# Performance work log

Hardware: AMD Instinct MI355X
Metric: run time of the kernel (lower is better)

Reference implementation:

```python
import jax, jax.numpy as jnp
import numpy as np

ALPHA = 1.5      # entmax alpha (q parameter)
N_ITER = 50      # entmax-bisect iterations (entmax library default)
B, S, DM, H, HKV, HD = 1, 2048, 2048, 16, 4, 128
ROPE_THETA = 10000.0


def _entmax_p(x):
    """alpha-entmax along last axis via bisection on tau (matches entmax.EntmaxBisect)."""
    am1 = ALPHA - 1.0
    pw = 1.0 / am1
    X = x * am1
    d = x.shape[-1]
    max_val = jnp.max(X, axis=-1, keepdims=True)
    tau_lo = max_val - 1.0                      # _gp(1, alpha) = 1
    tau_hi = max_val - (1.0 / d) ** am1          # _gp(1/d, alpha)
    dm0 = tau_hi - tau_lo

    def body(i, carry):
        tau_lo, dm, tau_m = carry
        dm = dm * 0.5
        tau_m = tau_lo + dm
        p = jnp.maximum(X - tau_m, 0.0) ** pw
        f = jnp.sum(p, axis=-1, keepdims=True) - 1.0
        tau_lo = jnp.where(f >= 0, tau_m, tau_lo)
        return (tau_lo, dm, tau_m)

    tau_lo, dm, tau_m = jax.lax.fori_loop(0, N_ITER, body, (tau_lo, dm0, tau_lo))
    p = jnp.maximum(X - tau_m, 0.0) ** pw
    return p / jnp.sum(p, axis=-1, keepdims=True)  # ensure_sum_one


@jax.custom_vjp
def entmax_bisect(x):
    return _entmax_p(x)

def _emx_fwd(x):
    p = _entmax_p(x)
    return p, p

def _emx_bwd(p, g):
    # entmax library backward: gppr = p^(2-alpha) on support
    gppr = jnp.where(p > 0, p ** (2.0 - ALPHA), 0.0)
    dX = g * gppr
    q = jnp.sum(dX, axis=-1, keepdims=True) / jnp.sum(gppr, axis=-1, keepdims=True)
    return ((dX - q * gppr),)

entmax_bisect.defvjp(_emx_fwd, _emx_bwd)


def _rotate_half(x):
    x1, x2 = x[..., : HD // 2], x[..., HD // 2:]
    return jnp.concatenate([-x2, x1], axis=-1)


def setup_inputs() -> dict:
    key = jax.random.key(0)
    k1, k2, k3, k4, k5 = jax.random.split(key, 5)
    hidden_states = jax.random.normal(k1, (B, S, DM), dtype=jnp.float32)
    wq = jax.random.normal(k2, (H * HD, DM), dtype=jnp.float32) * 0.02
    wk = jax.random.normal(k3, (HKV * HD, DM), dtype=jnp.float32) * 0.02
    wv = jax.random.normal(k4, (HKV * HD, DM), dtype=jnp.float32) * 0.02
    wo = jax.random.normal(k5, (DM, H * HD), dtype=jnp.float32) * 0.02
    # real Llama RoPE position embeddings
    inv_freq = 1.0 / (ROPE_THETA ** (np.arange(0, HD, 2, dtype=np.float32) / HD))
    pos = np.arange(S, dtype=np.float32)
    freqs = pos[:, None] * inv_freq[None, :]          # [S, HD/2]
    emb = np.concatenate([freqs, freqs], axis=-1)     # [S, HD]
    cos = jnp.asarray(np.cos(emb))[None]              # [1, S, HD]
    sin = jnp.asarray(np.sin(emb))[None]
    return {"hidden_states": hidden_states, "cos": cos, "sin": sin,
            "wq": wq, "wk": wk, "wv": wv, "wo": wo}


def reference(hidden_states, cos, sin, wq, wk, wv, wo):
    b, s, _ = hidden_states.shape
    scaling = HD ** -0.5
    # QKV projections -> [B, H, S, HD]
    q = (hidden_states @ wq.T).reshape(b, s, H, HD).transpose(0, 2, 1, 3)
    k = (hidden_states @ wk.T).reshape(b, s, HKV, HD).transpose(0, 2, 1, 3)
    v = (hidden_states @ wv.T).reshape(b, s, HKV, HD).transpose(0, 2, 1, 3)
    # RoPE (cos/sin broadcast over head axis)
    c, sn = cos[:, None, :, :], sin[:, None, :, :]
    q = q * c + _rotate_half(q) * sn
    k = k * c + _rotate_half(k) * sn
    # GQA: repeat kv heads
    g = H // HKV
    k = jnp.repeat(k, g, axis=1)
    v = jnp.repeat(v, g, axis=1)
    scores = jnp.einsum('bhqd,bhkd->bhqk', q, k) * scaling
    causal = jnp.tril(jnp.ones((s, s), dtype=bool))
    scores = jnp.where(causal, scores, -jnp.inf)
    attn = entmax_bisect(scores)                      # [B, H, S, S]
    out = jnp.einsum('bhqk,bhkd->bhqd', attn, v)
    out = out.transpose(0, 2, 1, 3).reshape(b, s, H * HD)
    out = out @ wo.T
    return (out, attn)
```

## Files before the change

### kernel.cpp

```cpp
#include <hip/hip_runtime.h>

typedef __bf16 bf16;
typedef __bf16 bf16x4 __attribute__((ext_vector_type(4)));
typedef __bf16 bf16x8 __attribute__((ext_vector_type(8)));
typedef float f32x4 __attribute__((ext_vector_type(4)));

#define S 2048
#define DM 2048
#define HD 128
#define H 16
#define NQKV 3072
#define N_ITER_DEV 32

__device__ __forceinline__ void gl2lds16(const void* g, void* l) {
    __builtin_amdgcn_global_load_lds(
        (const __attribute__((address_space(1))) void*)g,
        (__attribute__((address_space(3))) void*)l, 16, 0, 0);
}

__global__ void cvt4_kernel(const float* __restrict__ in, bf16* __restrict__ out, int n4) {
    int i = blockIdx.x * blockDim.x + threadIdx.x;
    if (i < n4) {
        float4 f = ((const float4*)in)[i];
        bf16x4 o;
        o[0] = (bf16)f.x; o[1] = (bf16)f.y; o[2] = (bf16)f.z; o[3] = (bf16)f.w;
        ((bf16x4*)out)[i] = o;
    }
}

__global__ __launch_bounds__(256) void gemm128_bt(const bf16* __restrict__ A,
                                                  const bf16* __restrict__ B,
                                                  float* __restrict__ C, int Ndim, int K) {
    __shared__ bf16 As[128 * 32];
    __shared__ bf16 Bs[128 * 32];
    int m0 = blockIdx.x * 128, n0 = blockIdx.y * 128;
    int t = threadIdx.x;
    int l = t & 63, w = t >> 6;
    int lane16 = l & 15, quad = l >> 4;

    int c0 = (w * 2) * 64 + l;
    int c1 = c0 + 64;
    const bf16* Abase = A + (size_t)m0 * K;
    const bf16* Bbase = B + (size_t)n0 * K;

    int wm = (w & 1) * 64, wn = (w >> 1) * 64;
    f32x4 acc[4][4];
#pragma unroll
    for (int i = 0; i < 4; i++)
#pragma unroll
        for (int j = 0; j < 4; j++) acc[i][j] = (f32x4){0.f, 0.f, 0.f, 0.f};

    for (int k0 = 0; k0 < K; k0 += 32) {
        gl2lds16(Abase + (size_t)(c0 >> 2) * K + k0 + (c0 & 3) * 8, &As[(w * 2) * 512]);
        gl2lds16(Abase + (size_t)(c1 >> 2) * K + k0 + (c1 & 3) * 8, &As[(w * 2 + 1) * 512]);
        gl2lds16(Bbase + (size_t)(c0 >> 2) * K + k0 + (c0 & 3) * 8, &Bs[(w * 2) * 512]);
        gl2lds16(Bbase + (size_t)(c1 >> 2) * K + k0 + (c1 & 3) * 8, &Bs[(w * 2 + 1) * 512]);
        __syncthreads();
        bf16x8 af[4], bfr[4];
#pragma unroll
        for (int i = 0; i < 4; i++)
            af[i] = *(const bf16x8*)&As[(wm + i * 16 + lane16) * 32 + quad * 8];
#pragma unroll
        for (int j = 0; j < 4; j++)
            bfr[j] = *(const bf16x8*)&Bs[(wn + j * 16 + lane16) * 32 + quad * 8];
#pragma unroll
        for (int i = 0; i < 4; i++)
#pragma unroll
            for (int j = 0; j < 4; j++)
                acc[i][j] = __builtin_amdgcn_mfma_f32_16x16x32_bf16(af[i], bfr[j], acc[i][j], 0, 0, 0);
        __syncthreads();
    }
#pragma unroll
    for (int i = 0; i < 4; i++)
#pragma unroll
        for (int j = 0; j < 4; j++) {
            float* cp = C + (size_t)(m0 + wm + i * 16 + quad * 4) * Ndim + n0 + wn + j * 16 + lane16;
#pragma unroll
            for (int r = 0; r < 4; r++) cp[(size_t)r * Ndim] = acc[i][j][r];
        }
}

__global__ void rope_kernel(const float* __restrict__ qkv, const float* __restrict__ cosb,
                            const float* __restrict__ sinb, bf16* __restrict__ qs,
                            bf16* __restrict__ kb, bf16* __restrict__ vT) {
    int col = blockIdx.x * 256 + threadIdx.x;
    int s = blockIdx.y;
    const float* row = qkv + (size_t)s * NQKV;
    float v = row[col];
    if (col < DM) {
        int h = col >> 7, d = col & 127;
        float c = cosb[s * HD + d], sn = sinb[s * HD + d];
        float other = row[(h << 7) + ((d < 64) ? (d + 64) : (d - 64))];
        float rot = (d < 64) ? -other : other;
        float o = v * c + rot * sn;
        qs[((size_t)h * S + s) * HD + d] = (bf16)(o * 0.04419417382415922f);
    } else if (col < DM + 512) {
        int c2 = col - DM;
        int kv = c2 >> 7, d = c2 & 127;
        float c = cosb[s * HD + d], sn = sinb[s * HD + d];
        float other = row[DM + (kv << 7) + ((d < 64) ? (d + 64) : (d - 64))];
        float rot = (d < 64) ? -other : other;
        float o = v * c + rot * sn;
        kb[((size_t)kv * S + s) * HD + d] = (bf16)o;
    } else {
        int c2 = col - DM - 512;
        int kv = c2 >> 7, d = c2 & 127;
        vT[((size_t)kv * HD + d) * S + s] = (bf16)v;
    }
}

template <int SEGS>
__global__ __launch_bounds__(1024) void attn_kernel(const bf16* __restrict__ qs,
                                                    const bf16* __restrict__ kb,
                                                    float* __restrict__ attn, int bx_base) {
    constexpr int NREG = SEGS * 8;
    __shared__ float sc[16][528];
    int bx = bx_base + blockIdx.x;
    int h = blockIdx.y;
    int r0 = bx * 16;
    int jlen = r0 + 16;
    int l = threadIdx.x & 63;
    int w = threadIdx.x >> 6;
    int lane16 = l & 15, quad = l >> 4;

    const bf16* qrow = qs + ((size_t)h * S + (r0 + lane16)) * HD + quad * 8;
    bf16x8 afrag[4];
#pragma unroll
    for (int kc = 0; kc < 4; kc++) afrag[kc] = *(const bf16x8*)(qrow + kc * 32);

    const bf16* kbase = kb + (size_t)(h >> 2) * S * HD;
    float xr[NREG];
    int my_i = r0 + w;

#pragma unroll
    for (int sgi = 0; sgi < SEGS; sgi++) {
        int j0 = sgi * 512;
#pragma unroll
        for (int tt = 0; tt < 2; tt++) {
            int t = w + tt * 16;
            int jt = j0 + t * 16;
            if (jt < jlen) {
                f32x4 acc = {0.f, 0.f, 0.f, 0.f};
                const bf16* kp = kbase + (size_t)(jt + lane16) * HD + quad * 8;
#pragma unroll
                for (int kc = 0; kc < 4; kc++) {
                    bf16x8 b = *(const bf16x8*)(kp + kc * 32);
                    acc = __builtin_amdgcn_mfma_f32_16x16x32_bf16(afrag[kc], b, acc, 0, 0, 0);
                }
                int jj = jt + lane16;
#pragma unroll
                for (int r = 0; r < 4; r++) {
                    int rowi = quad * 4 + r;
                    float v = acc[r];
                    if (jj > r0 + rowi) v = -1e30f;
                    sc[rowi][t * 16 + lane16] = v;
                }
            }
        }
        __syncthreads();
#pragma unroll
        for (int c = 0; c < 8; c++) {
            int j = j0 + c * 64 + l;
            xr[sgi * 8 + c] = (j < jlen) ? sc[w][c * 64 + l] : -1e30f;
        }
        __syncthreads();
    }

    float m = -1e30f;
#pragma unroll
    for (int c = 0; c < NREG; c++) m = fmaxf(m, xr[c]);
#pragma unroll
    for (int off = 1; off < 64; off <<= 1) m = fmaxf(m, __shfl_xor(m, off));

    float tau_lo = m - 1.0f;
    float dm = 0.97790291309f;
    float tau_m = tau_lo;
    for (int it = 0; it < N_ITER_DEV; it++) {
        dm *= 0.5f;
        tau_m = tau_lo + dm;
        float f = 0.f;
#pragma unroll
        for (int c = 0; c < NREG; c++) {
            float t = fmaxf(xr[c] - tau_m, 0.f);
            f = fmaf(t, t, f);
        }
#pragma unroll
        for (int off = 1; off < 64; off <<= 1) f += __shfl_xor(f, off);
        tau_lo = (f >= 1.0f) ? tau_m : tau_lo;
    }

    float ssum = 0.f;
#pragma unroll
    for (int c = 0; c < NREG; c++) {
        float t = fmaxf(xr[c] - tau_m, 0.f);
        ssum = fmaf(t, t, ssum);
    }
#pragma unroll
    for (int off = 1; off < 64; off <<= 1) ssum += __shfl_xor(ssum, off);
    float inv = 1.0f / ssum;

    float* arow = attn + ((size_t)h * S + my_i) * S;
#pragma unroll
    for (int c = 0; c < NREG; c++) {
        float t = fmaxf(xr[c] - tau_m, 0.f);
        arow[c * 64 + l] = t * t * inv;
    }
    for (int j = SEGS * 512 + l; j < S; j += 64) arow[j] = 0.f;
}

__global__ __launch_bounds__(256) void av128(const float* __restrict__ attn,
                                             const bf16* __restrict__ vT,
                                             bf16* __restrict__ o) {
    __shared__ bf16 As[64 * 32];
    __shared__ bf16 Bs[128 * 32];
    int m0 = blockIdx.x * 64;
    int h = blockIdx.y;
    int t = threadIdx.x, l = t & 63, w = t >> 6;
    int lane16 = l & 15, quad = l >> 4;
    const float* Abase = attn + ((size_t)h * S + m0) * S;
    const bf16* Bbase = vT + (size_t)(h >> 2) * HD * S;
    int wm = (w & 1) * 32, wn = (w >> 1) * 64;
    f32x4 acc[2][4];
#pragma unroll
    for (int i = 0; i < 2; i++)
#pragma unroll
        for (int j = 0; j < 4; j++) acc[i][j] = (f32x4){0.f, 0.f, 0.f, 0.f};

    int ar = t >> 2, ac = (t & 3) * 8;
    int cB0 = (w * 2) * 64 + l, cB1 = cB0 + 64;
    int Kv = m0 + 64;

    for (int k0 = 0; k0 < Kv; k0 += 32) {
        float4 f0 = *(const float4*)(Abase + (size_t)ar * S + k0 + ac);
        float4 f1 = *(const float4*)(Abase + (size_t)ar * S + k0 + ac + 4);
        bf16x8 a8;
        a8[0] = (bf16)f0.x; a8[1] = (bf16)f0.y; a8[2] = (bf16)f0.z; a8[3] = (bf16)f0.w;
        a8[4] = (bf16)f1.x; a8[5] = (bf16)f1.y; a8[6] = (bf16)f1.z; a8[7] = (bf16)f1.w;
        *(bf16x8*)&As[ar * 32 + ac] = a8;
        gl2lds16(Bbase + (size_t)(cB0 >> 2) * S + k0 + (cB0 & 3) * 8, &Bs[(w * 2) * 512]);
        gl2lds16(Bbase + (size_t)(cB1 >> 2) * S + k0 + (cB1 & 3) * 8, &Bs[(w * 2 + 1) * 512]);
        __syncthreads();
        bf16x8 af[2], bfr[4];
#pragma unroll
        for (int i = 0; i < 2; i++)
            af[i] = *(const bf16x8*)&As[(wm + i * 16 + lane16) * 32 + quad * 8];
#pragma unroll
        for (int j = 0; j < 4; j++)
            bfr[j] = *(const bf16x8*)&Bs[(wn + j * 16 + lane16) * 32 + quad * 8];
#pragma unroll
        for (int i = 0; i < 2; i++)
#pragma unroll
            for (int j = 0; j < 4; j++)
                acc[i][j] = __builtin_amdgcn_mfma_f32_16x16x32_bf16(af[i], bfr[j], acc[i][j], 0, 0, 0);
        __syncthreads();
    }
#pragma unroll
    for (int i = 0; i < 2; i++)
#pragma unroll
        for (int j = 0; j < 4; j++) {
            bf16* op = o + (size_t)(m0 + wm + i * 16 + quad * 4) * DM + h * HD + wn + j * 16 + lane16;
#pragma unroll
            for (int r = 0; r < 4; r++) op[(size_t)r * DM] = (bf16)acc[i][j][r];
        }
}

extern "C" void kernel_launch(void* const* d_in, const int* in_sizes, int n_in,
                              void* d_out, int out_size, void* d_ws, size_t ws_size,
                              hipStream_t stream) {
    const float* hidden = (const float*)d_in[0];
    const float* cosb   = (const float*)d_in[1];
    const float* sinb   = (const float*)d_in[2];
    const float* wq     = (const float*)d_in[3];
    const float* wk     = (const float*)d_in[4];
    const float* wv     = (const float*)d_in[5];
    const float* wo     = (const float*)d_in[6];
    char* ws = (char*)d_ws;
    bf16*  bf_hidden = (bf16*)(ws);
    bf16*  bf_wqkv   = (bf16*)(ws + 8388608);
    bf16*  bf_wo     = (bf16*)(ws + 20971520);
    float* qkv_raw   = (float*)(ws + 29360128);
    bf16*  qsb       = (bf16*)(ws + 54525952);
    bf16*  kbb       = (bf16*)(ws + 62914560);
    bf16*  vTb       = (bf16*)(ws + 65011712);
    float* out  = (float*)d_out;
    float* attn = out + 4194304;

    cvt4_kernel<<<dim3(4096), 256, 0, stream>>>(hidden, bf_hidden, 1048576);
    cvt4_kernel<<<dim3(4096), 256, 0, stream>>>(wq, bf_wqkv, 1048576);
    cvt4_kernel<<<dim3(1024), 256, 0, stream>>>(wk, bf_wqkv + 2048 * 2048, 262144);
    cvt4_kernel<<<dim3(1024), 256, 0, stream>>>(wv, bf_wqkv + 2048 * 2048 + 512 * 2048, 262144);
    cvt4_kernel<<<dim3(4096), 256, 0, stream>>>(wo, bf_wo, 1048576);

    gemm128_bt<<<dim3(16, 24), 256, 0, stream>>>(bf_hidden, bf_wqkv, qkv_raw, NQKV, DM);

    rope_kernel<<<dim3(12, S), 256, 0, stream>>>(qkv_raw, cosb, sinb, qsb, kbb, vTb);

    attn_kernel<1><<<dim3(32, H), 1024, 0, stream>>>(qsb, kbb, attn, 0);
    attn_kernel<2><<<dim3(32, H), 1024, 0, stream>>>(qsb, kbb, attn, 32);
    attn_kernel<3><<<dim3(32, H), 1024, 0, stream>>>(qsb, kbb, attn, 64);
    attn_kernel<4><<<dim3(32, H), 1024, 0, stream>>>(qsb, kbb, attn, 96);

    av128<<<dim3(32, H), 256, 0, stream>>>(attn, vTb, bf_hidden);

    gemm128_bt<<<dim3(16, 16), 256, 0, stream>>>(bf_hidden, bf_wo, out, DM, DM);
}
```

Before: 693.9 us.

## Fuse attention-times-V into entmax attention kernel and merge conversion launches

```diff
diff --git a/kernel.cpp b/kernel.cpp
--- a/kernel.cpp
+++ b/kernel.cpp
@@ -18,14 +18,23 @@
         (__attribute__((address_space(3))) void*)l, 16, 0, 0);
 }
 
-__global__ void cvt4_kernel(const float* __restrict__ in, bf16* __restrict__ out, int n4) {
+__global__ void cvt_all(const float* __restrict__ hid, const float* __restrict__ wq,
+                        const float* __restrict__ wk, const float* __restrict__ wv,
+                        const float* __restrict__ wo, bf16* __restrict__ bh,
+                        bf16* __restrict__ bqkv, bf16* __restrict__ bwo) {
     int i = blockIdx.x * blockDim.x + threadIdx.x;
-    if (i < n4) {
-        float4 f = ((const float4*)in)[i];
-        bf16x4 o;
-        o[0] = (bf16)f.x; o[1] = (bf16)f.y; o[2] = (bf16)f.z; o[3] = (bf16)f.w;
-        ((bf16x4*)out)[i] = o;
-    }
+    const float* src;
+    bf16* dst;
+    int off;
+    if (i < 1048576) { src = hid; dst = bh; off = i; }
+    else if (i < 2097152) { src = wq; dst = bqkv; off = i - 1048576; }
+    else if (i < 2359296) { src = wk; dst = bqkv + 2048 * 2048; off = i - 2097152; }
+    else if (i < 2621440) { src = wv; dst = bqkv + 2048 * 2048 + 512 * 2048; off = i - 2359296; }
+    else { src = wo; dst = bwo; off = i - 2621440; }
+    float4 f = ((const float4*)src)[off];
+    bf16x4 o;
+    o[0] = (bf16)f.x; o[1] = (bf16)f.y; o[2] = (bf16)f.z; o[3] = (bf16)f.w;
+    ((bf16x4*)dst)[off] = o;
 }
 
 __global__ __launch_bounds__(256) void gemm128_bt(const bf16* __restrict__ A,
@@ -110,11 +119,14 @@
 }
 
 template <int SEGS>
-__global__ __launch_bounds__(1024) void attn_kernel(const bf16* __restrict__ qs,
-                                                    const bf16* __restrict__ kb,
-                                                    float* __restrict__ attn, int bx_base) {
+__global__ __launch_bounds__(1024) void attn_av_kernel(const bf16* __restrict__ qs,
+                                                       const bf16* __restrict__ kb,
+                                                       const bf16* __restrict__ vT,
+                                                       float* __restrict__ attn,
+                                                       bf16* __restrict__ o, int bx_base) {
     constexpr int NREG = SEGS * 8;
     __shared__ float sc[16][528];
+    __shared__ bf16 pb[16][552];
     int bx = bx_base + blockIdx.x;
     int h = blockIdx.y;
     int r0 = bx * 16;
@@ -129,6 +141,7 @@
     for (int kc = 0; kc < 4; kc++) afrag[kc] = *(const bf16x8*)(qrow + kc * 32);
 
     const bf16* kbase = kb + (size_t)(h >> 2) * S * HD;
+    const bf16* vbase = vT + (size_t)(h >> 2) * HD * S;
     float xr[NREG];
     int my_i = r0 + w;
 
@@ -173,11 +186,11 @@
     for (int off = 1; off < 64; off <<= 1) m = fmaxf(m, __shfl_xor(m, off));
 
     float tau_lo = m - 1.0f;
-    float dm = 0.97790291309f;
+    float dmh = 0.97790291309f;
     float tau_m = tau_lo;
     for (int it = 0; it < N_ITER_DEV; it++) {
-        dm *= 0.5f;
-        tau_m = tau_lo + dm;
+        dmh *= 0.5f;
+        tau_m = tau_lo + dmh;
         float f = 0.f;
 #pragma unroll
         for (int c = 0; c < NREG; c++) {
@@ -200,68 +213,46 @@
     float inv = 1.0f / ssum;
 
     float* arow = attn + ((size_t)h * S + my_i) * S;
-#pragma unroll
-    for (int c = 0; c < NREG; c++) {
-        float t = fmaxf(xr[c] - tau_m, 0.f);
-        arow[c * 64 + l] = t * t * inv;
-    }
+    int jt_o = (w & 7) * 16;
+    int kh = (w >> 3) * 256;
+    f32x4 acc_o = {0.f, 0.f, 0.f, 0.f};
+
+#pragma unroll
+    for (int sgi = 0; sgi < SEGS; sgi++) {
+        int j0 = sgi * 512;
+#pragma unroll
+        for (int c = 0; c < 8; c++) {
+            float t = fmaxf(xr[sgi * 8 + c] - tau_m, 0.f);
+            float p = t * t * inv;
+            arow[j0 + c * 64 + l] = p;
+            pb[w][c * 64 + l] = (bf16)p;
+        }
+        __syncthreads();
+#pragma unroll
+        for (int ks = 0; ks < 8; ks++) {
+            int kk = kh + ks * 32;
+            bf16x8 a = *(const bf16x8*)&pb[lane16][kk + quad * 8];
+            bf16x8 b = *(const bf16x8*)(vbase + (size_t)(jt_o + lane16) * S + j0 + kk + quad * 8);
+            acc_o = __builtin_amdgcn_mfma_f32_16x16x32_bf16(a, b, acc_o, 0, 0, 0);
+        }
+        __syncthreads();
+    }
+
     for (int j = SEGS * 512 + l; j < S; j += 64) arow[j] = 0.f;
-}
-
-__global__ __launch_bounds__(256) void av128(const float* __restrict__ attn,
-                                             const bf16* __restrict__ vT,
-                                             bf16* __restrict__ o) {
-    __shared__ bf16 As[64 * 32];
-    __shared__ bf16 Bs[128 * 32];
-    int m0 = blockIdx.x * 64;
-    int h = blockIdx.y;
-    int t = threadIdx.x, l = t & 63, w = t >> 6;
-    int lane16 = l & 15, quad = l >> 4;
-    const float* Abase = attn + ((size_t)h * S + m0) * S;
-    const bf16* Bbase = vT + (size_t)(h >> 2) * HD * S;
-    int wm = (w & 1) * 32, wn = (w >> 1) * 64;
-    f32x4 acc[2][4];
-#pragma unroll
-    for (int i = 0; i < 2; i++)
-#pragma unroll
-        for (int j = 0; j < 4; j++) acc[i][j] = (f32x4){0.f, 0.f, 0.f, 0.f};
-
-    int ar = t >> 2, ac = (t & 3) * 8;
-    int cB0 = (w * 2) * 64 + l, cB1 = cB0 + 64;
-    int Kv = m0 + 64;
-
-    for (int k0 = 0; k0 < Kv; k0 += 32) {
-        float4 f0 = *(const float4*)(Abase + (size_t)ar * S + k0 + ac);
-        float4 f1 = *(const float4*)(Abase + (size_t)ar * S + k0 + ac + 4);
-        bf16x8 a8;
-        a8[0] = (bf16)f0.x; a8[1] = (bf16)f0.y; a8[2] = (bf16)f0.z; a8[3] = (bf16)f0.w;
-        a8[4] = (bf16)f1.x; a8[5] = (bf16)f1.y; a8[6] = (bf16)f1.z; a8[7] = (bf16)f1.w;
-        *(bf16x8*)&As[ar * 32 + ac] = a8;
-        gl2lds16(Bbase + (size_t)(cB0 >> 2) * S + k0 + (cB0 & 3) * 8, &Bs[(w * 2) * 512]);
-        gl2lds16(Bbase + (size_t)(cB1 >> 2) * S + k0 + (cB1 & 3) * 8, &Bs[(w * 2 + 1) * 512]);
-        __syncthreads();
-        bf16x8 af[2], bfr[4];
-#pragma unroll
-        for (int i = 0; i < 2; i++)
-            af[i] = *(const bf16x8*)&As[(wm + i * 16 + lane16) * 32 + quad * 8];
-#pragma unroll
-        for (int j = 0; j < 4; j++)
-            bfr[j] = *(const bf16x8*)&Bs[(wn + j * 16 + lane16) * 32 + quad * 8];
-#pragma unroll
-        for (int i = 0; i < 2; i++)
-#pragma unroll
-            for (int j = 0; j < 4; j++)
-                acc[i][j] = __builtin_amdgcn_mfma_f32_16x16x32_bf16(af[i], bfr[j], acc[i][j], 0, 0, 0);
-        __syncthreads();
-    }
-#pragma unroll
-    for (int i = 0; i < 2; i++)
-#pragma unroll
-        for (int j = 0; j < 4; j++) {
-            bf16* op = o + (size_t)(m0 + wm + i * 16 + quad * 4) * DM + h * HD + wn + j * 16 + lane16;
-#pragma unroll
-            for (int r = 0; r < 4; r++) op[(size_t)r * DM] = (bf16)acc[i][j][r];
-        }
+
+    if (w >= 8) {
+#pragma unroll
+        for (int r = 0; r < 4; r++) sc[w - 8][l * 4 + r] = acc_o[r];
+    }
+    __syncthreads();
+    if (w < 8) {
+        bf16* op = o + (size_t)(r0 + quad * 4) * DM + h * HD + jt_o + lane16;
+#pragma unroll
+        for (int r = 0; r < 4; r++) {
+            float v = acc_o[r] + sc[w][l * 4 + r];
+            op[(size_t)r * DM] = (bf16)v;
+        }
+    }
 }
 
 extern "C" void kernel_launch(void* const* d_in, const int* in_sizes, int n_in,
@@ -285,22 +276,16 @@
     float* out  = (float*)d_out;
     float* attn = out + 4194304;
 
-    cvt4_kernel<<<dim3(4096), 256, 0, stream>>>(hidden, bf_hidden, 1048576);
-    cvt4_kernel<<<dim3(4096), 256, 0, stream>>>(wq, bf_wqkv, 1048576);
-    cvt4_kernel<<<dim3(1024), 256, 0, stream>>>(wk, bf_wqkv + 2048 * 2048, 262144);
-    cvt4_kernel<<<dim3(1024), 256, 0, stream>>>(wv, bf_wqkv + 2048 * 2048 + 512 * 2048, 262144);
-    cvt4_kernel<<<dim3(4096), 256, 0, stream>>>(wo, bf_wo, 1048576);
+    cvt_all<<<dim3(14336), 256, 0, stream>>>(hidden, wq, wk, wv, wo, bf_hidden, bf_wqkv, bf_wo);
 
     gemm128_bt<<<dim3(16, 24), 256, 0, stream>>>(bf_hidden, bf_wqkv, qkv_raw, NQKV, DM);
 
     rope_kernel<<<dim3(12, S), 256, 0, stream>>>(qkv_raw, cosb, sinb, qsb, kbb, vTb);
 
-    attn_kernel<1><<<dim3(32, H), 1024, 0, stream>>>(qsb, kbb, attn, 0);
-    attn_kernel<2><<<dim3(32, H), 1024, 0, stream>>>(qsb, kbb, attn, 32);
-    attn_kernel<3><<<dim3(32, H), 1024, 0, stream>>>(qsb, kbb, attn, 64);
-    attn_kernel<4><<<dim3(32, H), 1024, 0, stream>>>(qsb, kbb, attn, 96);
-
-    av128<<<dim3(32, H), 256, 0, stream>>>(attn, vTb, bf_hidden);
+    attn_av_kernel<1><<<dim3(32, H), 1024, 0, stream>>>(qsb, kbb, vTb, attn, bf_hidden, 0);
+    attn_av_kernel<2><<<dim3(32, H), 1024, 0, stream>>>(qsb, kbb, vTb, attn, bf_hidden, 32);
+    attn_av_kernel<3><<<dim3(32, H), 1024, 0, stream>>>(qsb, kbb, vTb, attn, bf_hidden, 64);
+    attn_av_kernel<4><<<dim3(32, H), 1024, 0, stream>>>(qsb, kbb, vTb, attn, bf_hidden, 96);
 
     gemm128_bt<<<dim3(16, 16), 256, 0, stream>>>(bf_hidden, bf_wo, out, DM, DM);
 }
```

New measurement: 689.2 us. No clear change (-0.7%).
